# Performance work log

Measured on AMD Instinct MI355X. Metric: run time of the kernel, lower is better.

## Reference

```python
import jax, jax.numpy as jnp
import numpy as np
import math

IN_FEATURES = 4096
OUT_FEATURES = 4096
N_ROWS = 8192
EPS = 1e-6
ROOT2 = math.sqrt(2.0)


def setup_inputs() -> dict:
    key = jax.random.key(0)
    k1, k2 = jax.random.split(key)
    # p_x: probabilities in [0,1]
    p_x = jax.random.uniform(k1, (N_ROWS, IN_FEATURES), dtype=jnp.float32)
    # weight ~ Uniform(-2, 2) per reset_parameters
    weight = jax.random.uniform(k2, (OUT_FEATURES, IN_FEATURES), dtype=jnp.float32, minval=-2.0, maxval=2.0)
    return {"p_x": p_x, "weight": weight}


def reference(p_x, weight):
    in_features = weight.shape[1]
    threshold = -(-in_features // 2)  # ceil(in_features / 2)
    p_w = jax.nn.sigmoid(weight)  # (O, I)
    # p_success = 2*p_w*p_x + 1 - p_x - p_w = c*p_x + d, with:
    c = 2.0 * p_w - 1.0          # (O, I)
    d = 1.0 - p_w                # (O, I)
    # mu = sum_i p_success = p_x @ c^T + sum_i d   -- never materialize (..., O, I)
    mu = jnp.einsum('ni,oi->no', p_x, c) + jnp.sum(d, axis=-1)  # (N, O)
    # sum_i p_success^2 = p_x^2 @ (c^2)^T + 2 * p_x @ (c*d)^T + sum_i d^2
    sum_sq = (jnp.einsum('ni,oi->no', p_x * p_x, c * c)
              + 2.0 * jnp.einsum('ni,oi->no', p_x, c * d)
              + jnp.sum(d * d, axis=-1))  # (N, O)
    # sum p_success*(1 - p_success) = mu - sum_sq
    sigma = jnp.sqrt(mu - sum_sq + EPS)  # (N, O)
    p_actives = 0.5 - 0.5 * jax.lax.erf((threshold - 0.5 - mu) / (sigma * ROOT2))
    return p_actives
```

## Files before the change

### kernel.cpp

```cpp
#include <hip/hip_runtime.h>
#include <hip/hip_bf16.h>
#include <math.h>
#include <cstdint>

#define KDIM 4096
#define ODIM 4096
#define MDIM 8192
#define EPSF 1e-6f
#define TM05 2047.5f

typedef __bf16 bf16x8 __attribute__((ext_vector_type(8)));
typedef float f32x4 __attribute__((ext_vector_type(4)));
typedef unsigned short u16;

#define XY_DELTA (MDIM * KDIM)
#define CD_DELTA (ODIM * KDIM)

#define VSTRIDE 132

__device__ __forceinline__ u16 f2bf(float f) {
  __hip_bfloat16 h = __float2bfloat16(f);
  return __builtin_bit_cast(u16, h);
}
__device__ __forceinline__ float bf2f(u16 b) {
  unsigned int u = ((unsigned int)b) << 16;
  return __builtin_bit_cast(float, u);
}

__device__ __forceinline__ void async_cp16(void* lds, const void* g) {
  __builtin_amdgcn_global_load_lds(
      (__attribute__((address_space(1))) void*)(uintptr_t)g,
      (__attribute__((address_space(3))) void*)lds, 16, 0, 0);
}

__global__ void prep_x_kernel(const float4* __restrict__ x4,
                              ushort4* __restrict__ Xb,
                              ushort4* __restrict__ Yb) {
  int i = blockIdx.x * blockDim.x + threadIdx.x;
  float4 v = x4[i];
  ushort4 xo, yo;
  xo.x = f2bf(v.x); xo.y = f2bf(v.y); xo.z = f2bf(v.z); xo.w = f2bf(v.w);
  yo.x = f2bf(v.x * (1.0f - v.x));
  yo.y = f2bf(v.y * (1.0f - v.y));
  yo.z = f2bf(v.z * (1.0f - v.z));
  yo.w = f2bf(v.w * (1.0f - v.w));
  Xb[i] = xo;
  Yb[i] = yo;
}

__device__ __forceinline__ void wcomp(float w, u16& cb, u16& c2b, float& sd, float& sde) {
  float pw = 1.0f / (1.0f + __expf(-w));
  float c  = 2.0f * pw - 1.0f;
  float d  = 1.0f - pw;
  cb  = f2bf(c);
  c2b = f2bf(c * c);
  sd  += d;
  sde += d * pw;
}

__global__ void prep_w_kernel(const float4* __restrict__ w4,
                              ushort4* __restrict__ Cb,
                              ushort4* __restrict__ C2b,
                              float* __restrict__ sumd,
                              float* __restrict__ sumde) {
  const int o = blockIdx.x;
  const int t = threadIdx.x;
  const float4* wr = w4 + (size_t)o * (KDIM / 4);
  ushort4* cr  = Cb  + (size_t)o * (KDIM / 4);
  ushort4* c2r = C2b + (size_t)o * (KDIM / 4);
  float sd = 0.f, sde = 0.f;
#pragma unroll
  for (int it = 0; it < KDIM / 4 / 256; ++it) {
    int k4 = t + it * 256;
    float4 w = wr[k4];
    ushort4 co, c2o;
    wcomp(w.x, co.x, c2o.x, sd, sde);
    wcomp(w.y, co.y, c2o.y, sd, sde);
    wcomp(w.z, co.z, c2o.z, sd, sde);
    wcomp(w.w, co.w, c2o.w, sd, sde);
    cr[k4]  = co;
    c2r[k4] = c2o;
  }
#pragma unroll
  for (int off = 32; off > 0; off >>= 1) {
    sd  += __shfl_down(sd, off);
    sde += __shfl_down(sde, off);
  }
  __shared__ float red[8];
  if ((t & 63) == 0) { red[t >> 6] = sd; red[4 + (t >> 6)] = sde; }
  __syncthreads();
  if (t == 0) {
    sumd[o]  = red[0] + red[1] + red[2] + red[3];
    sumde[o] = red[4] + red[5] + red[6] + red[7];
  }
}

__global__ __launch_bounds__(512, 4) void gemm_fused_kernel(
    const u16* __restrict__ Xb, const u16* __restrict__ Cb,
    const float* __restrict__ sumd, const float* __restrict__ sumde,
    float* __restrict__ out) {
  __shared__ __attribute__((aligned(16))) u16 smem[128 * VSTRIDE];

  const int tid  = threadIdx.x;
  const int lane = tid & 63;
  const int wave = tid >> 6;
  const int grp  = wave >> 2;
  const int sub  = wave & 3;
  const int wm   = sub >> 1;
  const int wn   = sub & 1;
  const int quad = lane >> 4;
  const int r16  = lane & 15;

  const int m0 = blockIdx.y * 128;
  const int n0 = blockIdx.x * 128;

  const int srow = tid >> 2;
  const int c    = tid & 3;
  const int scol = (c ^ ((srow >> 1) & 3)) * 8;
  const u16* gA = Xb + (size_t)(m0 + srow) * KDIM + scol;
  const u16* gB = Cb + (size_t)(n0 + srow) * KDIM + scol;
  u16* ls = smem + tid * 8;

  f32x4 acc[4][4];
#pragma unroll
  for (int i = 0; i < 4; ++i)
#pragma unroll
    for (int j = 0; j < 4; ++j) acc[i][j] = f32x4{0.f, 0.f, 0.f, 0.f};

  const u16* aT = smem + grp * 4096;
  const u16* bT = smem + 8192 + grp * 4096;

  const int swz  = (quad ^ ((r16 >> 1) & 3)) * 8;
  const int aoff = (wm * 64 + r16) * 32 + swz;
  const int boff = (wn * 64 + r16) * 32 + swz;

  for (int kt = 0; kt < KDIM / 32; ++kt) {
    const int kk = kt * 32;
    async_cp16(ls,        gA + kk);
    async_cp16(ls + 4096, gA + kk + XY_DELTA);
    async_cp16(ls + 8192, gB + kk);
    async_cp16(ls + 12288, gB + kk + CD_DELTA);
    __syncthreads();

    bf16x8 a[4], b[4];
#pragma unroll
    for (int i = 0; i < 4; ++i) a[i] = *(const bf16x8*)(aT + aoff + i * 16 * 32);
#pragma unroll
    for (int j = 0; j < 4; ++j) b[j] = *(const bf16x8*)(bT + boff + j * 16 * 32);
#pragma unroll
    for (int i = 0; i < 4; ++i)
#pragma unroll
      for (int j = 0; j < 4; ++j)
        acc[i][j] = __builtin_amdgcn_mfma_f32_16x16x32_bf16(a[i], b[j], acc[i][j], 0, 0, 0);
    __syncthreads();
  }

  if (grp) {
#pragma unroll
    for (int j = 0; j < 4; ++j) {
      const int cl = wn * 64 + j * 16 + r16;
#pragma unroll
      for (int i = 0; i < 4; ++i) {
        const int rl = wm * 64 + i * 16 + quad * 4;
        f32x4 v = acc[i][j];
        ushort4 p;
        p.x = f2bf(v[0]); p.y = f2bf(v[1]); p.z = f2bf(v[2]); p.w = f2bf(v[3]);
        *(ushort4*)(smem + cl * VSTRIDE + rl) = p;
      }
    }
  }
  __syncthreads();
  if (!grp) {
    const float inv_rt2 = 0.70710678118654752f;
#pragma unroll
    for (int j = 0; j < 4; ++j) {
      const int cl  = wn * 64 + j * 16 + r16;
      const int col = n0 + cl;
      const float sd  = sumd[col];
      const float sde = sumde[col] + EPSF;
#pragma unroll
      for (int i = 0; i < 4; ++i) {
        const int rl   = wm * 64 + i * 16 + quad * 4;
        const int mrow = m0 + rl;
        const ushort4 p = *(const ushort4*)(smem + cl * VSTRIDE + rl);
        f32x4 m4 = acc[i][j];
        const float vv[4] = {bf2f(p.x), bf2f(p.y), bf2f(p.z), bf2f(p.w)};
#pragma unroll
        for (int r = 0; r < 4; ++r) {
          float mu  = m4[r] + sd;
          float var = vv[r] + sde;
          float z = (TM05 - mu) * rsqrtf(var) * inv_rt2;
          out[(size_t)(mrow + r) * ODIM + col] = 0.5f * erfcf(z);
        }
      }
    }
  }
}

extern "C" void kernel_launch(void* const* d_in, const int* in_sizes, int n_in,
                              void* d_out, int out_size, void* d_ws, size_t ws_size,
                              hipStream_t stream) {
  const float* p_x    = (const float*)d_in[0];
  const float* weight = (const float*)d_in[1];
  float* out = (float*)d_out;
  char* ws = (char*)d_ws;

  u16* Cb      = (u16*)(ws);
  float* sumd  = (float*)(ws + 67108864);
  float* sumde = (float*)(ws + 67125248);
  u16* Xb      = (u16*)(ws + 67141632);

  prep_w_kernel<<<ODIM, 256, 0, stream>>>((const float4*)weight, (ushort4*)Cb,
                                          (ushort4*)(ws + 33554432), sumd, sumde);
  prep_x_kernel<<<(MDIM * KDIM / 4) / 256, 256, 0, stream>>>((const float4*)p_x,
                                                             (ushort4*)Xb,
                                                             (ushort4*)(ws + 134250496));
  dim3 grid(ODIM / 128, MDIM / 128);
  gemm_fused_kernel<<<grid, 512, 0, stream>>>(Xb, Cb, sumd, sumde, out);
}
```

Before: 944.8 us.

## Triple-buffer LDS pipeline with 128x256 tiles and XCD-aware block remapping

Reworks the fused dual-GEMM main loop. Tiles grow from 128x128 to 128x256, and LDS becomes a three-stage ring buffer that async-loads the tiles two steps ahead. Each K step is split into two halves with prefetches interleaved between the MFMA groups, plus setprio and explicit vmcnt waits in place of full syncthreads. Block indices are remapped across the 8 XCDs for cache locality. This aims to hide global-load latency and raise arithmetic intensity, at the cost of more registers and LDS and lower occupancy (launch bounds drop to 2).

```diff
diff --git a/kernel.cpp b/kernel.cpp
--- a/kernel.cpp
+++ b/kernel.cpp
@@ -17,6 +17,16 @@
 #define CD_DELTA (ODIM * KDIM)
 
 #define VSTRIDE 132
+
+#define BM 128
+#define BN 256
+#define BK 32
+#define NT (KDIM / BK)
+#define BUF_BYTES 49152
+#define LX_OFF 0
+#define LY_OFF 8192
+#define LC_OFF 16384
+#define LD_OFF 32768
 
 __device__ __forceinline__ u16 f2bf(float f) {
   __hip_bfloat16 h = __float2bfloat16(f);
@@ -95,77 +105,122 @@
   }
 }
 
-__global__ __launch_bounds__(512, 4) void gemm_fused_kernel(
+__global__ __launch_bounds__(512, 2) void gemm_fused_kernel(
     const u16* __restrict__ Xb, const u16* __restrict__ Cb,
     const float* __restrict__ sumd, const float* __restrict__ sumde,
     float* __restrict__ out) {
-  __shared__ __attribute__((aligned(16))) u16 smem[128 * VSTRIDE];
+  __shared__ __attribute__((aligned(128))) char smem[3 * BUF_BYTES];
 
   const int tid  = threadIdx.x;
   const int lane = tid & 63;
   const int wave = tid >> 6;
   const int grp  = wave >> 2;
   const int sub  = wave & 3;
-  const int wm   = sub >> 1;
-  const int wn   = sub & 1;
+  const int wr   = sub >> 1;
+  const int wc   = sub & 1;
   const int quad = lane >> 4;
   const int r16  = lane & 15;
 
-  const int m0 = blockIdx.y * 128;
-  const int n0 = blockIdx.x * 128;
-
-  const int srow = tid >> 2;
-  const int c    = tid & 3;
-  const int scol = (c ^ ((srow >> 1) & 3)) * 8;
-  const u16* gA = Xb + (size_t)(m0 + srow) * KDIM + scol;
-  const u16* gB = Cb + (size_t)(n0 + srow) * KDIM + scol;
-  u16* ls = smem + tid * 8;
-
-  f32x4 acc[4][4];
+  const int raw = blockIdx.x;
+  const int wg  = (raw & 7) * 128 + (raw >> 3);
+  const int n0  = (wg >> 6) * BN;
+  const int m0  = (wg & 63) * BM;
+
+  const int su    = tid >> 3;
+  const int sg    = (tid & 7) ^ (su & 7);
+  const int srow  = 2 * su + (sg >> 2);
+  const int selem = (sg & 3) * 8;
+
+  const u16* gX = Xb + (size_t)(m0 + srow) * KDIM + selem;
+  const u16* gC = Cb + (size_t)(n0 + srow) * KDIM + selem;
+
+#define STAGE_A(sbuf, kt) do {                                              \
+    char* _d = smem + (sbuf) * BUF_BYTES + tid * 16;                        \
+    const u16* _px = gX + (size_t)(kt) * BK;                                \
+    const u16* _pc = gC + (size_t)(kt) * BK;                                \
+    async_cp16(_d + LX_OFF, _px);                                           \
+    async_cp16(_d + LY_OFF, _px + XY_DELTA);                                \
+    async_cp16(_d + LC_OFF, _pc);                                           \
+  } while (0)
+#define STAGE_B(sbuf, kt) do {                                              \
+    char* _d = smem + (sbuf) * BUF_BYTES + tid * 16;                        \
+    const u16* _pc = gC + (size_t)(kt) * BK;                                \
+    async_cp16(_d + LC_OFF + 8192, _pc + (size_t)128 * KDIM);               \
+    async_cp16(_d + LD_OFF,        _pc + CD_DELTA);                         \
+    async_cp16(_d + LD_OFF + 8192, _pc + CD_DELTA + (size_t)128 * KDIM);    \
+  } while (0)
+
+  const int rh    = r16 >> 1;
+  const int fbase = rh * 128 + (((((r16 & 1) << 2) + quad) ^ rh) << 4);
+  const int aT = (grp ? LY_OFF : LX_OFF) + wr * 4096 + fbase;
+  const int bT = (grp ? LD_OFF : LC_OFF) + wc * 8192 + fbase;
+
+  f32x4 acc[4][8];
 #pragma unroll
   for (int i = 0; i < 4; ++i)
 #pragma unroll
-    for (int j = 0; j < 4; ++j) acc[i][j] = f32x4{0.f, 0.f, 0.f, 0.f};
-
-  const u16* aT = smem + grp * 4096;
-  const u16* bT = smem + 8192 + grp * 4096;
-
-  const int swz  = (quad ^ ((r16 >> 1) & 3)) * 8;
-  const int aoff = (wm * 64 + r16) * 32 + swz;
-  const int boff = (wn * 64 + r16) * 32 + swz;
-
-  for (int kt = 0; kt < KDIM / 32; ++kt) {
-    const int kk = kt * 32;
-    async_cp16(ls,        gA + kk);
-    async_cp16(ls + 4096, gA + kk + XY_DELTA);
-    async_cp16(ls + 8192, gB + kk);
-    async_cp16(ls + 12288, gB + kk + CD_DELTA);
-    __syncthreads();
-
-    bf16x8 a[4], b[4];
-#pragma unroll
-    for (int i = 0; i < 4; ++i) a[i] = *(const bf16x8*)(aT + aoff + i * 16 * 32);
-#pragma unroll
-    for (int j = 0; j < 4; ++j) b[j] = *(const bf16x8*)(bT + boff + j * 16 * 32);
+    for (int j = 0; j < 8; ++j) acc[i][j] = f32x4{0.f, 0.f, 0.f, 0.f};
+
+  STAGE_A(0, 0); STAGE_B(0, 0);
+  STAGE_A(1, 1); STAGE_B(1, 1);
+  asm volatile("s_waitcnt vmcnt(6)" ::: "memory");
+  __builtin_amdgcn_s_barrier();
+
+  int rb = 0;
+  for (int t = 0; t < NT; ++t) {
+    const char* base = smem + rb * BUF_BYTES;
+    const int sb = rb ? rb - 1 : 2;
+    bf16x8 a[4], b[8];
+
+#pragma unroll
+    for (int i = 0; i < 4; ++i) a[i] = *(const bf16x8*)(base + aT + i * 1024);
+#pragma unroll
+    for (int j = 0; j < 4; ++j) b[j] = *(const bf16x8*)(base + bT + j * 1024);
+    if (t + 2 < NT) STAGE_A(sb, t + 2);
+    __builtin_amdgcn_s_barrier();
+    asm volatile("s_waitcnt lgkmcnt(0)" ::: "memory");
+    __builtin_amdgcn_sched_barrier(0);
+    __builtin_amdgcn_s_setprio(1);
 #pragma unroll
     for (int i = 0; i < 4; ++i)
 #pragma unroll
       for (int j = 0; j < 4; ++j)
         acc[i][j] = __builtin_amdgcn_mfma_f32_16x16x32_bf16(a[i], b[j], acc[i][j], 0, 0, 0);
-    __syncthreads();
-  }
-
+    __builtin_amdgcn_s_setprio(0);
+    __builtin_amdgcn_s_barrier();
+
+#pragma unroll
+    for (int j = 4; j < 8; ++j) b[j] = *(const bf16x8*)(base + bT + j * 1024);
+    if (t + 2 < NT) STAGE_B(sb, t + 2);
+    __builtin_amdgcn_s_barrier();
+    asm volatile("s_waitcnt lgkmcnt(0)" ::: "memory");
+    __builtin_amdgcn_sched_barrier(0);
+    __builtin_amdgcn_s_setprio(1);
+#pragma unroll
+    for (int i = 0; i < 4; ++i)
+#pragma unroll
+      for (int j = 4; j < 8; ++j)
+        acc[i][j] = __builtin_amdgcn_mfma_f32_16x16x32_bf16(a[i], b[j], acc[i][j], 0, 0, 0);
+    __builtin_amdgcn_s_setprio(0);
+    if (t < NT - 2) { asm volatile("s_waitcnt vmcnt(6)" ::: "memory"); }
+    else            { asm volatile("s_waitcnt vmcnt(0)" ::: "memory"); }
+    __builtin_amdgcn_s_barrier();
+
+    rb = rb + 1 == 3 ? 0 : rb + 1;
+  }
+
+  u16* vb = (u16*)smem;
   if (grp) {
 #pragma unroll
-    for (int j = 0; j < 4; ++j) {
-      const int cl = wn * 64 + j * 16 + r16;
+    for (int j = 0; j < 8; ++j) {
+      const int cl = wc * 128 + j * 16 + r16;
 #pragma unroll
       for (int i = 0; i < 4; ++i) {
-        const int rl = wm * 64 + i * 16 + quad * 4;
+        const int rl = wr * 64 + i * 16 + quad * 4;
         f32x4 v = acc[i][j];
         ushort4 p;
         p.x = f2bf(v[0]); p.y = f2bf(v[1]); p.z = f2bf(v[2]); p.w = f2bf(v[3]);
-        *(ushort4*)(smem + cl * VSTRIDE + rl) = p;
+        *(ushort4*)(vb + cl * VSTRIDE + rl) = p;
       }
     }
   }
@@ -173,16 +228,16 @@
   if (!grp) {
     const float inv_rt2 = 0.70710678118654752f;
 #pragma unroll
-    for (int j = 0; j < 4; ++j) {
-      const int cl  = wn * 64 + j * 16 + r16;
+    for (int j = 0; j < 8; ++j) {
+      const int cl  = wc * 128 + j * 16 + r16;
       const int col = n0 + cl;
       const float sd  = sumd[col];
       const float sde = sumde[col] + EPSF;
 #pragma unroll
       for (int i = 0; i < 4; ++i) {
-        const int rl   = wm * 64 + i * 16 + quad * 4;
+        const int rl   = wr * 64 + i * 16 + quad * 4;
         const int mrow = m0 + rl;
-        const ushort4 p = *(const ushort4*)(smem + cl * VSTRIDE + rl);
+        const ushort4 p = *(const ushort4*)(vb + cl * VSTRIDE + rl);
         f32x4 m4 = acc[i][j];
         const float vv[4] = {bf2f(p.x), bf2f(p.y), bf2f(p.z), bf2f(p.w)};
 #pragma unroll
@@ -215,6 +270,6 @@
   prep_x_kernel<<<(MDIM * KDIM / 4) / 256, 256, 0, stream>>>((const float4*)p_x,
                                                              (ushort4*)Xb,
                                                              (ushort4*)(ws + 134250496));
-  dim3 grid(ODIM / 128, MDIM / 128);
-  gemm_fused_kernel<<<grid, 512, 0, stream>>>(Xb, Cb, sumd, sumde, out);
-}
+  gemm_fused_kernel<<<dim3((ODIM / BN) * (MDIM / BM)), 512, 0, stream>>>(
+      Xb, Cb, sumd, sumde, out);
+}
```

Result: no change. 949.0 us (+0.4%).

## Split fused dual GEMM into two 256x256-tile passes with double-buffered LDS pipeline

Applied to the files above, without the earlier changes.

Replaces the single fused kernel, which computed both GEMMs at 128x128 tiles with half the block per product, with two launches of a 256x256-tile kernel. Each launch stages 64-wide K slices into double-buffered LDS, interleaves async loads with MFMA phases using explicit waitcnt, barriers and setprio, and remaps workgroup IDs for L2 locality. The first pass writes the variance GEMM result to the output buffer in fp32, and the second reads it back to apply the erfc epilogue. This raises MFMA reuse per LDS byte and overlaps loads with compute, at the cost of an extra full fp32 write and read of the output and an extra launch.

```diff
diff --git a/kernel.cpp b/kernel.cpp
--- a/kernel.cpp
+++ b/kernel.cpp
@@ -16,7 +16,7 @@
 #define XY_DELTA (MDIM * KDIM)
 #define CD_DELTA (ODIM * KDIM)
 
-#define VSTRIDE 132
+#define NITER (KDIM / 128)
 
 __device__ __forceinline__ u16 f2bf(float f) {
   __hip_bfloat16 h = __float2bfloat16(f);
@@ -95,102 +95,137 @@
   }
 }
 
-__global__ __launch_bounds__(512, 4) void gemm_fused_kernel(
-    const u16* __restrict__ Xb, const u16* __restrict__ Cb,
+
+#define STG_H(bb, isB, half, srcB, tt) do {                                    \
+    char* _d = smem + (bb) * 65536 + (isB) * 32768 + (half) * 16384 + tid * 16;\
+    const u16* _s = (srcB) + (size_t)((half) * 128) * KDIM + (size_t)(tt) * 64;\
+    async_cp16(_d, _s);                                                        \
+    async_cp16(_d + 8192, _s + (size_t)64 * KDIM);                             \
+  } while (0)
+
+#define PHASE(bb, p, STG, VM) {                                                \
+    const char* Ab = smem + (bb) * 65536;                                      \
+    const char* Bb = Ab + 32768;                                               \
+    bf16x8 a0k0 = *(const bf16x8*)(Ab + arow + ((p) * 2 + 0) * 2048 + g0);     \
+    bf16x8 a0k1 = *(const bf16x8*)(Ab + arow + ((p) * 2 + 0) * 2048 + g1);     \
+    bf16x8 a1k0 = *(const bf16x8*)(Ab + arow + ((p) * 2 + 1) * 2048 + g0);     \
+    bf16x8 a1k1 = *(const bf16x8*)(Ab + arow + ((p) * 2 + 1) * 2048 + g1);     \
+    if ((p) == 0) {                                                            \
+      _Pragma("unroll") for (int j = 0; j < 4; ++j) {                          \
+        b0[j] = *(const bf16x8*)(Bb + brow + j * 2048 + g0);                   \
+        b1[j] = *(const bf16x8*)(Bb + brow + j * 2048 + g1);                   \
+      }                                                                        \
+    }                                                                          \
+    STG;                                                                       \
+    __builtin_amdgcn_s_barrier();                                              \
+    asm volatile("s_waitcnt lgkmcnt(0)" ::: "memory");                         \
+    __builtin_amdgcn_sched_barrier(0);                                         \
+    __builtin_amdgcn_s_setprio(1);                                             \
+    _Pragma("unroll") for (int j = 0; j < 4; ++j)                              \
+      acc[(p)*2+0][j] = __builtin_amdgcn_mfma_f32_16x16x32_bf16(a0k0, b0[j], acc[(p)*2+0][j], 0, 0, 0); \
+    _Pragma("unroll") for (int j = 0; j < 4; ++j)                              \
+      acc[(p)*2+1][j] = __builtin_amdgcn_mfma_f32_16x16x32_bf16(a1k0, b0[j], acc[(p)*2+1][j], 0, 0, 0); \
+    _Pragma("unroll") for (int j = 0; j < 4; ++j)                              \
+      acc[(p)*2+0][j] = __builtin_amdgcn_mfma_f32_16x16x32_bf16(a0k1, b1[j], acc[(p)*2+0][j], 0, 0, 0); \
+    _Pragma("unroll") for (int j = 0; j < 4; ++j)                              \
+      acc[(p)*2+1][j] = __builtin_amdgcn_mfma_f32_16x16x32_bf16(a1k1, b1[j], acc[(p)*2+1][j], 0, 0, 0); \
+    __builtin_amdgcn_s_setprio(0);                                             \
+    VM;                                                                        \
+    __builtin_amdgcn_s_barrier();                                              \
+  }
+
+template <int PASS>
+__global__ __launch_bounds__(512, 2) void gemm_pass_kernel(
+    const u16* __restrict__ Ag, const u16* __restrict__ Bg,
     const float* __restrict__ sumd, const float* __restrict__ sumde,
     float* __restrict__ out) {
-  __shared__ __attribute__((aligned(16))) u16 smem[128 * VSTRIDE];
+  __shared__ __attribute__((aligned(128))) char smem[2 * 65536];
 
   const int tid  = threadIdx.x;
   const int lane = tid & 63;
   const int wave = tid >> 6;
-  const int grp  = wave >> 2;
-  const int sub  = wave & 3;
-  const int wm   = sub >> 1;
-  const int wn   = sub & 1;
+  const int wr   = wave >> 2;
+  const int wc   = wave & 3;
   const int quad = lane >> 4;
   const int r16  = lane & 15;
 
-  const int m0 = blockIdx.y * 128;
-  const int n0 = blockIdx.x * 128;
-
-  const int srow = tid >> 2;
-  const int c    = tid & 3;
-  const int scol = (c ^ ((srow >> 1) & 3)) * 8;
-  const u16* gA = Xb + (size_t)(m0 + srow) * KDIM + scol;
-  const u16* gB = Cb + (size_t)(n0 + srow) * KDIM + scol;
-  u16* ls = smem + tid * 8;
-
-  f32x4 acc[4][4];
-#pragma unroll
-  for (int i = 0; i < 4; ++i)
+  const int raw = blockIdx.x;
+  const int wg  = (raw & 7) * 64 + (raw >> 3);
+  const int n0  = (wg >> 5) * 256;
+  const int m0  = (wg & 31) * 256;
+
+  const int srow = tid >> 3;
+  const int scol = ((tid & 7) ^ (srow & 7)) * 8;
+  const u16* gA = Ag + (size_t)(m0 + srow) * KDIM + scol;
+  const u16* gB = Bg + (size_t)(n0 + srow) * KDIM + scol;
+
+  const int r7   = r16 & 7;
+  const int g0   = (quad ^ r7) * 16;
+  const int g1   = ((4 | quad) ^ r7) * 16;
+  const int arow = (wr * 128 + r16) * 128;
+  const int brow = (wc * 64 + r16) * 128;
+
+  f32x4 acc[8][4];
+#pragma unroll
+  for (int i = 0; i < 8; ++i)
 #pragma unroll
     for (int j = 0; j < 4; ++j) acc[i][j] = f32x4{0.f, 0.f, 0.f, 0.f};
 
-  const u16* aT = smem + grp * 4096;
-  const u16* bT = smem + 8192 + grp * 4096;
-
-  const int swz  = (quad ^ ((r16 >> 1) & 3)) * 8;
-  const int aoff = (wm * 64 + r16) * 32 + swz;
-  const int boff = (wn * 64 + r16) * 32 + swz;
-
-  for (int kt = 0; kt < KDIM / 32; ++kt) {
-    const int kk = kt * 32;
-    async_cp16(ls,        gA + kk);
-    async_cp16(ls + 4096, gA + kk + XY_DELTA);
-    async_cp16(ls + 8192, gB + kk);
-    async_cp16(ls + 12288, gB + kk + CD_DELTA);
-    __syncthreads();
-
-    bf16x8 a[4], b[4];
-#pragma unroll
-    for (int i = 0; i < 4; ++i) a[i] = *(const bf16x8*)(aT + aoff + i * 16 * 32);
-#pragma unroll
-    for (int j = 0; j < 4; ++j) b[j] = *(const bf16x8*)(bT + boff + j * 16 * 32);
-#pragma unroll
-    for (int i = 0; i < 4; ++i)
-#pragma unroll
-      for (int j = 0; j < 4; ++j)
-        acc[i][j] = __builtin_amdgcn_mfma_f32_16x16x32_bf16(a[i], b[j], acc[i][j], 0, 0, 0);
-    __syncthreads();
-  }
-
-  if (grp) {
+  bf16x8 b0[4], b1[4];
+
+  STG_H(0, 0, 0, gA, 0); STG_H(0, 0, 1, gA, 0);
+  STG_H(0, 1, 0, gB, 0); STG_H(0, 1, 1, gB, 0);
+  STG_H(1, 1, 0, gB, 1); STG_H(1, 1, 1, gB, 1);
+  asm volatile("s_waitcnt vmcnt(4)" ::: "memory");
+  __builtin_amdgcn_s_barrier();
+
+  for (int s = 0; s < NITER; ++s) {
+    const bool nlast = (s + 1 < NITER);
+    const int t1 = 2 * s + 1, t2 = 2 * s + 2, t3 = 2 * s + 3;
+
+    PHASE(0, 0, STG_H(1, 0, 0, gA, t1), )
+    PHASE(0, 1, STG_H(1, 0, 1, gA, t1), )
+    PHASE(0, 2, if (nlast) STG_H(0, 1, 0, gB, t2), )
+    PHASE(0, 3, if (nlast) STG_H(0, 1, 1, gB, t2),
+          if (nlast) { asm volatile("s_waitcnt vmcnt(4)" ::: "memory"); }
+          else       { asm volatile("s_waitcnt vmcnt(0)" ::: "memory"); })
+    PHASE(1, 0, if (nlast) STG_H(0, 0, 0, gA, t2), )
+    PHASE(1, 1, if (nlast) STG_H(0, 0, 1, gA, t2), )
+    PHASE(1, 2, if (nlast) STG_H(1, 1, 0, gB, t3), )
+    PHASE(1, 3, if (nlast) STG_H(1, 1, 1, gB, t3),
+          if (nlast) { asm volatile("s_waitcnt vmcnt(4)" ::: "memory"); }
+          else       { asm volatile("s_waitcnt vmcnt(0)" ::: "memory"); })
+  }
+
+  if (PASS == 0) {
 #pragma unroll
     for (int j = 0; j < 4; ++j) {
-      const int cl = wn * 64 + j * 16 + r16;
-#pragma unroll
-      for (int i = 0; i < 4; ++i) {
-        const int rl = wm * 64 + i * 16 + quad * 4;
+      const int col = n0 + wc * 64 + j * 16 + r16;
+#pragma unroll
+      for (int i = 0; i < 8; ++i) {
+        const int row = m0 + wr * 128 + i * 16 + quad * 4;
         f32x4 v = acc[i][j];
-        ushort4 p;
-        p.x = f2bf(v[0]); p.y = f2bf(v[1]); p.z = f2bf(v[2]); p.w = f2bf(v[3]);
-        *(ushort4*)(smem + cl * VSTRIDE + rl) = p;
+#pragma unroll
+        for (int r = 0; r < 4; ++r) out[(size_t)(row + r) * ODIM + col] = v[r];
       }
     }
-  }
-  __syncthreads();
-  if (!grp) {
+  } else {
     const float inv_rt2 = 0.70710678118654752f;
 #pragma unroll
     for (int j = 0; j < 4; ++j) {
-      const int cl  = wn * 64 + j * 16 + r16;
-      const int col = n0 + cl;
+      const int col = n0 + wc * 64 + j * 16 + r16;
       const float sd  = sumd[col];
       const float sde = sumde[col] + EPSF;
 #pragma unroll
-      for (int i = 0; i < 4; ++i) {
-        const int rl   = wm * 64 + i * 16 + quad * 4;
-        const int mrow = m0 + rl;
-        const ushort4 p = *(const ushort4*)(smem + cl * VSTRIDE + rl);
+      for (int i = 0; i < 8; ++i) {
+        const int row = m0 + wr * 128 + i * 16 + quad * 4;
         f32x4 m4 = acc[i][j];
-        const float vv[4] = {bf2f(p.x), bf2f(p.y), bf2f(p.z), bf2f(p.w)};
 #pragma unroll
         for (int r = 0; r < 4; ++r) {
+          float var = out[(size_t)(row + r) * ODIM + col] + sde;
           float mu  = m4[r] + sd;
-          float var = vv[r] + sde;
           float z = (TM05 - mu) * rsqrtf(var) * inv_rt2;
-          out[(size_t)(mrow + r) * ODIM + col] = 0.5f * erfcf(z);
+          out[(size_t)(row + r) * ODIM + col] = 0.5f * erfcf(z);
         }
       }
     }
@@ -206,15 +241,18 @@
   char* ws = (char*)d_ws;
 
   u16* Cb      = (u16*)(ws);
+  u16* C2b     = (u16*)(ws + 33554432);
   float* sumd  = (float*)(ws + 67108864);
   float* sumde = (float*)(ws + 67125248);
   u16* Xb      = (u16*)(ws + 67141632);
+  u16* Yb      = (u16*)(ws + 134250496);
 
   prep_w_kernel<<<ODIM, 256, 0, stream>>>((const float4*)weight, (ushort4*)Cb,
-                                          (ushort4*)(ws + 33554432), sumd, sumde);
+                                          (ushort4*)C2b, sumd, sumde);
   prep_x_kernel<<<(MDIM * KDIM / 4) / 256, 256, 0, stream>>>((const float4*)p_x,
                                                              (ushort4*)Xb,
-                                                             (ushort4*)(ws + 134250496));
-  dim3 grid(ODIM / 128, MDIM / 128);
-  gemm_fused_kernel<<<grid, 512, 0, stream>>>(Xb, Cb, sumd, sumde, out);
-}
+                                                             (ushort4*)Yb);
+  const int nwg = (MDIM / 256) * (ODIM / 256);
+  gemm_pass_kernel<0><<<nwg, 512, 0, stream>>>(Yb, C2b, sumd, sumde, out);
+  gemm_pass_kernel<1><<<nwg, 512, 0, stream>>>(Xb, Cb, sumd, sumde, out);
+}
```

New measurement: 774.3 us. 18.0% less time.
